# Kernel optimization log

Hardware: AMD Instinct MI355X
Metric: run time of the kernel (lower is better)

Reference implementation:

```python
import jax, jax.numpy as jnp
import numpy as np

B, N, D, D_OUT = 8, 2048, 1024, 1024

def setup_inputs() -> dict:
    key = jax.random.key(0)
    k1, k2, k3, k4, k5 = jax.random.split(key, 5)
    x = jax.random.normal(k1, (B, N, D), dtype=jnp.float32)
    # nn.Linear params: weight [out, in], bias [out]
    W_attn = jax.random.normal(k2, (D, D), dtype=jnp.float32) / np.sqrt(D)
    b_attn = jax.random.normal(k3, (D,), dtype=jnp.float32) * 0.01
    W_out = jax.random.normal(k4, (D_OUT, D), dtype=jnp.float32) / np.sqrt(D)
    b_out = jax.random.normal(k5, (D_OUT,), dtype=jnp.float32) * 0.01
    return {"x": x, "W_attn": W_attn, "b_attn": b_attn, "W_out": W_out, "b_out": b_out}

def reference(x, W_attn, b_attn, W_out, b_out):
    # query = x; key = attention_linear(x); value = output_linear(x)
    key = jnp.einsum('bnd,kd->bnk', x, W_attn) + b_attn   # [B,N,D]
    value = jnp.einsum('bnd,od->bno', x, W_out) + b_out   # [B,N,D_OUT]
    scale = 1.0 / np.sqrt(x.shape[-1]).astype(np.float32)
    scores = jnp.einsum('bqd,bkd->bqk', x, key) * scale   # [B,N,N]
    attn = jax.nn.softmax(scores, axis=-1)
    return jnp.einsum('bqk,bko->bqo', attn, value)        # [B,N,D_OUT]
```

## Files before the change

### kernel.cpp

```cpp
#include <hip/hip_runtime.h>
#include <hip/hip_bf16.h>
#include <cstdio>

typedef __bf16 bf16_t;
typedef __bf16 bf16x8 __attribute__((ext_vector_type(8)));
typedef __bf16 bf16x4 __attribute__((ext_vector_type(4)));
typedef float  f32x16 __attribute__((ext_vector_type(16)));

#define TM 128
#define TN 128
#define BK 32

__global__ __launch_bounds__(256)
void cvt_all(const float* __restrict__ x,  bf16_t* __restrict__ xb,  int nX,
             const float* __restrict__ Wa, bf16_t* __restrict__ Wab,
             const float* __restrict__ Wo, bf16_t* __restrict__ Wob, int nW)
{
    const int nT = nX + 2 * nW;
    for (int i = (blockIdx.x * 256 + threadIdx.x) * 4; i < nT; i += gridDim.x * 256 * 4) {
        const float* src; bf16_t* dst; int off;
        if (i < nX)            { src = x;  dst = xb;  off = i; }
        else if (i < nX + nW)  { src = Wa; dst = Wab; off = i - nX; }
        else                   { src = Wo; dst = Wob; off = i - nX - nW; }
        const float4 v = *(const float4*)(src + off);
        bf16x4 o;
        o[0] = (bf16_t)v.x; o[1] = (bf16_t)v.y; o[2] = (bf16_t)v.z; o[3] = (bf16_t)v.w;
        *(bf16x4*)(dst + off) = o;
    }
}

__device__ __forceinline__ void stage_tiles(
    const bf16_t* __restrict__ Ab, const bf16_t* __restrict__ Bb,
    bf16_t* As, bf16_t* Bs, int k0, int K, int t, int w)
{
    const int src_c = (t & 3) ^ ((t >> 3) & 3);
#pragma unroll
    for (int rd = 0; rd < 2; rd++) {
        const int row = rd * 64 + (t >> 2);
        __builtin_amdgcn_global_load_lds(
            (const __attribute__((address_space(1))) void*)(Ab + (size_t)row * K + k0 + src_c * 8),
            (__attribute__((address_space(3))) void*)(&As[(rd * 64 + w * 16) * 32]), 16, 0, 0);
        __builtin_amdgcn_global_load_lds(
            (const __attribute__((address_space(1))) void*)(Bb + (size_t)row * K + k0 + src_c * 8),
            (__attribute__((address_space(3))) void*)(&Bs[(rd * 64 + w * 16) * 32]), 16, 0, 0);
    }
}

__device__ __forceinline__ int fidx(int row, int c)
{
    return row * 32 + ((c ^ ((row >> 1) & 3)) * 8);
}

#define ACC_INIT(acc)                                            \
    _Pragma("unroll") for (int i = 0; i < 2; i++)                \
    _Pragma("unroll") for (int j = 0; j < 2; j++)                \
    _Pragma("unroll") for (int e = 0; e < 16; e++) acc[i][j][e] = 0.f;

#define MAINLOOP_STEP(As, Bs)                                                     \
    {                                                                             \
        bf16x8 af[2][2], bfr[2][2];                                               \
        _Pragma("unroll") for (int ks = 0; ks < 2; ks++) {                        \
            const int c = ks * 2 + lk;                                            \
            _Pragma("unroll") for (int mt = 0; mt < 2; mt++)                      \
                af[ks][mt] = *(const bf16x8*)&As[fidx(wm * 64 + mt * 32 + lm, c)];\
            _Pragma("unroll") for (int nt = 0; nt < 2; nt++)                      \
                bfr[ks][nt] = *(const bf16x8*)&Bs[fidx(wn * 64 + nt * 32 + lm, c)];\
        }                                                                         \
        _Pragma("unroll") for (int ks = 0; ks < 2; ks++)                          \
        _Pragma("unroll") for (int mt = 0; mt < 2; mt++)                          \
        _Pragma("unroll") for (int nt = 0; nt < 2; nt++)                          \
            acc[mt][nt] = __builtin_amdgcn_mfma_f32_32x32x16_bf16(                \
                af[ks][mt], bfr[ks][nt], acc[mt][nt], 0, 0, 0);                   \
    }

__global__ __launch_bounds__(256)
void gemm_scores(const bf16_t* __restrict__ A, const bf16_t* __restrict__ Bm,
                 bf16_t* __restrict__ C, float scale, int Ncols, int K,
                 long long strideA, long long strideB, long long strideC,
                 int tiles_m, int tiles_n)
{
    __shared__ bf16_t As[TM * BK];
    __shared__ bf16_t Bs[TN * BK];

    const int t    = threadIdx.x;
    const int w    = t >> 6;
    const int lane = t & 63;
    const int wm = w >> 1, wn = w & 1;
    const int lm = lane & 31;
    const int lk = lane >> 5;

    const int per_batch = tiles_m * tiles_n;
    const int batch = blockIdx.x / per_batch;
    const int rest  = blockIdx.x % per_batch;
    const int tm    = rest % tiles_m;
    const int tn    = rest / tiles_m;

    const bf16_t* Ab = A + (size_t)batch * strideA + (size_t)tm * TM * K;
    const bf16_t* Bb = Bm + (size_t)batch * strideB + (size_t)tn * TN * K;

    f32x16 acc[2][2];
    ACC_INIT(acc)

    for (int k0 = 0; k0 < K; k0 += BK) {
        stage_tiles(Ab, Bb, As, Bs, k0, K, t, w);
        __syncthreads();
        MAINLOOP_STEP(As, Bs)
        __syncthreads();
    }

#pragma unroll
    for (int mt = 0; mt < 2; mt++)
#pragma unroll
        for (int nt = 0; nt < 2; nt++) {
            const int colg = tn * TN + wn * 64 + nt * 32 + lm;
#pragma unroll
            for (int rg = 0; rg < 4; rg++) {
                const int rowg = tm * TM + wm * 64 + mt * 32 + rg * 8 + 4 * lk;
                bf16_t* p = C + (size_t)batch * strideC + (size_t)rowg * Ncols + colg;
#pragma unroll
                for (int j = 0; j < 4; j++)
                    p[(size_t)j * Ncols] = (bf16_t)(acc[mt][nt][rg * 4 + j] * scale);
            }
        }
}

__global__ __launch_bounds__(256)
void gemm_kv(const bf16_t* __restrict__ A,
             const bf16_t* __restrict__ Wa, const bf16_t* __restrict__ Wo,
             const float* __restrict__ ba, const float* __restrict__ bo,
             bf16_t* __restrict__ key, bf16_t* __restrict__ vT,
             int Nn, int Dd, int K)
{
    __shared__ bf16_t As[TM * BK];
    __shared__ bf16_t Bs[TN * BK];

    const int t    = threadIdx.x;
    const int w    = t >> 6;
    const int lane = t & 63;
    const int wm = w >> 1, wn = w & 1;
    const int lm = lane & 31;
    const int lk = lane >> 5;

    const int tiles_m = Nn / TM;
    const int per_batch = tiles_m * 16;
    const int batch = blockIdx.x / per_batch;
    const int rest  = blockIdx.x % per_batch;
    const int tm    = rest % tiles_m;
    const int tn    = rest / tiles_m;
    const bool isK  = (tn < 8);

    const bf16_t* Ab = A + (size_t)batch * Nn * K + (size_t)tm * TM * K;
    const bf16_t* Bb = (isK ? Wa + (size_t)tn * TN * K
                            : Wo + (size_t)(tn - 8) * TN * K);
    const float* bias = isK ? ba : bo;

    f32x16 acc[2][2];
    ACC_INIT(acc)

    for (int k0 = 0; k0 < K; k0 += BK) {
        stage_tiles(Ab, Bb, As, Bs, k0, K, t, w);
        __syncthreads();
        MAINLOOP_STEP(As, Bs)
        __syncthreads();
    }

#pragma unroll
    for (int mt = 0; mt < 2; mt++)
#pragma unroll
        for (int nt = 0; nt < 2; nt++) {
            const int cw = (tn & 7) * TN + wn * 64 + nt * 32 + lm;
            const float bv = bias[cw];
#pragma unroll
            for (int rg = 0; rg < 4; rg++) {
                const int rowg = tm * TM + wm * 64 + mt * 32 + rg * 8 + 4 * lk;
                if (isK) {
                    bf16_t* p = key + (size_t)batch * Nn * Dd + (size_t)rowg * Dd + cw;
#pragma unroll
                    for (int j = 0; j < 4; j++)
                        p[(size_t)j * Dd] = (bf16_t)(acc[mt][nt][rg * 4 + j] + bv);
                } else {
                    bf16_t* p = vT + (size_t)batch * Dd * Nn + (size_t)cw * Nn + rowg;
                    bf16x4 pk;
#pragma unroll
                    for (int j = 0; j < 4; j++)
                        pk[j] = (bf16_t)(acc[mt][nt][rg * 4 + j] + bv);
                    *(bf16x4*)p = pk;
                }
            }
        }
}

__global__ __launch_bounds__(256)
void softmax_rows(bf16_t* __restrict__ S)
{
    __shared__ float red[8];
    const int t = threadIdx.x;
    const int w = t >> 6;
    const int lane = t & 63;
    bf16_t* p = S + (size_t)blockIdx.x * 2048;

    bf16x8 v = *(const bf16x8*)&p[t * 8];
    float x[8];
    float m = -1e30f;
#pragma unroll
    for (int i = 0; i < 8; i++) { x[i] = (float)v[i]; m = fmaxf(m, x[i]); }
#pragma unroll
    for (int off = 32; off >= 1; off >>= 1) m = fmaxf(m, __shfl_xor(m, off));
    if (lane == 0) red[w] = m;
    __syncthreads();
    m = fmaxf(fmaxf(red[0], red[1]), fmaxf(red[2], red[3]));

    float s = 0.f;
#pragma unroll
    for (int i = 0; i < 8; i++) { x[i] = __expf(x[i] - m); s += x[i]; }
#pragma unroll
    for (int off = 32; off >= 1; off >>= 1) s += __shfl_xor(s, off);
    if (lane == 0) red[4 + w] = s;
    __syncthreads();
    const float inv = 1.f / (red[4] + red[5] + red[6] + red[7]);

    bf16x8 o;
#pragma unroll
    for (int i = 0; i < 8; i++) o[i] = (bf16_t)(x[i] * inv);
    *(bf16x8*)&p[t * 8] = o;
}

__global__ __launch_bounds__(256)
void gemm_out(const bf16_t* __restrict__ P, const bf16_t* __restrict__ vT,
              float* __restrict__ out, int Nn, int Dd)
{
    __shared__ bf16_t As[TM * BK];
    __shared__ bf16_t Bs[TN * BK];

    const int t    = threadIdx.x;
    const int w    = t >> 6;
    const int lane = t & 63;
    const int wm = w >> 1, wn = w & 1;
    const int lm = lane & 31;
    const int lk = lane >> 5;

    const int tiles_m = Nn / TM;
    const int tiles_n = Dd / TN;
    const int per_batch = tiles_m * tiles_n;
    const int batch = blockIdx.x / per_batch;
    const int rest  = blockIdx.x % per_batch;
    const int tm    = rest % tiles_m;
    const int tn    = rest / tiles_m;

    const int K = Nn;
    const bf16_t* Ab = P + (size_t)batch * Nn * Nn + (size_t)tm * TM * K;
    const bf16_t* Bb = vT + (size_t)batch * Dd * Nn + (size_t)tn * TN * K;

    f32x16 acc[2][2];
    ACC_INIT(acc)

    for (int k0 = 0; k0 < K; k0 += BK) {
        stage_tiles(Ab, Bb, As, Bs, k0, K, t, w);
        __syncthreads();
        MAINLOOP_STEP(As, Bs)
        __syncthreads();
    }

#pragma unroll
    for (int mt = 0; mt < 2; mt++)
#pragma unroll
        for (int nt = 0; nt < 2; nt++) {
            const int colg = tn * TN + wn * 64 + nt * 32 + lm;
#pragma unroll
            for (int rg = 0; rg < 4; rg++) {
                const int rowg = tm * TM + wm * 64 + mt * 32 + rg * 8 + 4 * lk;
                float* p = out + (size_t)batch * Nn * Dd + (size_t)rowg * Dd + colg;
#pragma unroll
                for (int j = 0; j < 4; j++)
                    p[(size_t)j * Dd] = acc[mt][nt][rg * 4 + j];
            }
        }
}

extern "C" void kernel_launch(void* const* d_in, const int* in_sizes, int n_in,
                              void* d_out, int out_size, void* d_ws, size_t ws_size,
                              hipStream_t stream)
{
    const int Bn = 8, Nn = 2048, Dd = 1024;

    const float* x  = (const float*)d_in[0];
    const float* Wa = (const float*)d_in[1];
    const float* ba = (const float*)d_in[2];
    const float* Wo = (const float*)d_in[3];
    const float* bo = (const float*)d_in[4];
    float* out = (float*)d_out;

    const size_t nX = (size_t)Bn * Nn * Dd;
    const size_t nW = (size_t)Dd * Dd;
    const size_t nS = (size_t)Bn * Nn * Nn;

    bf16_t* xb  = (bf16_t*)d_ws;
    bf16_t* Wab = xb + nX;
    bf16_t* Wob = Wab + nW;
    bf16_t* key = Wob + nW;
    bf16_t* vT  = key + nX;
    bf16_t* S   = vT + nX;
    const size_t needed = (nX * 3 + nW * 2 + nS) * sizeof(bf16_t);
    if (ws_size < needed)
        fprintf(stderr, "kernel_launch: ws too small: have %zu need %zu\n", ws_size, needed);

    const dim3 blk(256);
    const long long sXN = (long long)Nn * Dd;
    const long long sS  = (long long)Nn * Nn;

    cvt_all<<<dim3(18432), blk, 0, stream>>>(x, xb, (int)nX, Wa, Wab, Wo, Wob, (int)nW);

    gemm_kv<<<dim3(Bn * 16 * 16), blk, 0, stream>>>(
        xb, Wab, Wob, ba, bo, key, vT, Nn, Dd, Dd);

    gemm_scores<<<dim3(Bn * 16 * 16), blk, 0, stream>>>(
        xb, key, S, 0.03125f, Nn, Dd, sXN, sXN, sS, 16, 16);

    softmax_rows<<<dim3(Bn * Nn), blk, 0, stream>>>(S);

    gemm_out<<<dim3(Bn * 16 * 8), blk, 0, stream>>>(
        S, vT, out, Nn, Dd);
}
```

Before: 420.9 us.

## Replace 128x128 GEMMs with 256x256 tiled, double-buffered, 8-wave pipelined GEMM core

Rewrites the three GEMMs to use a shared 256x256-tile core with 512 threads, BK=64, double-buffered LDS fed by global_load_lds, and interleaved stage/compute phases with explicit waitcnt, barriers and setprio. Block indices are remapped to group tiles across XCDs. The intent is to raise arithmetic intensity and overlap global loads with MFMA work, cutting memory traffic and sync stalls. In exchange it uses far more LDS and registers, which limits occupancy, and launches fewer blocks (256 for the output GEMM), which may leave CUs idle.

```diff
diff --git a/kernel.cpp b/kernel.cpp
--- a/kernel.cpp
+++ b/kernel.cpp
@@ -7,9 +7,7 @@
 typedef __bf16 bf16x4 __attribute__((ext_vector_type(4)));
 typedef float  f32x16 __attribute__((ext_vector_type(16)));
 
-#define TM 128
-#define TN 128
-#define BK 32
+#define TILE_E (256 * 64)
 
 __global__ __launch_bounds__(256)
 void cvt_all(const float* __restrict__ x,  bf16_t* __restrict__ xb,  int nX,
@@ -29,165 +27,223 @@
     }
 }
 
-__device__ __forceinline__ void stage_tiles(
+
+template<int K>
+__device__ __forceinline__ void stage_half(
+    const bf16_t* __restrict__ src, bf16_t* lds_tile,
+    int half, int kt, int w, int l)
+{
+    const int r0 = half * 128 + w * 8 + (l >> 3);
+    const int c8 = ((l & 7) ^ (l >> 3)) * 8;
+#pragma unroll
+    for (int rr = 0; rr < 2; rr++) {
+        __builtin_amdgcn_global_load_lds(
+            (const __attribute__((address_space(1))) void*)
+                (src + (size_t)(r0 + rr * 64) * K + (size_t)kt * 64 + c8),
+            (__attribute__((address_space(3))) void*)
+                (lds_tile + (half * 128 + rr * 64 + w * 8) * 64),
+            16, 0, 0);
+    }
+}
+
+#define RDF_A(f, ks) (*(const bf16x8*)&sAc[(aoff + (f) * 32 + l31) * 64 + ((((ks) * 2 + l5) ^ lo7) * 8)])
+#define RDF_B(f, ks) (*(const bf16x8*)&sBc[(boff + (f) * 32 + l31) * 64 + ((((ks) * 2 + l5) ^ lo7) * 8)])
+
+#define MFMA_QUAD(BV, MB, NB)                                              \
+    _Pragma("unroll") for (int ks = 0; ks < 4; ks++)                       \
+    _Pragma("unroll") for (int mi = 0; mi < 2; mi++)                       \
+        acc[(MB) + mi][NB] = __builtin_amdgcn_mfma_f32_32x32x16_bf16(      \
+            ar[mi][ks], BV[ks], acc[(MB) + mi][NB], 0, 0, 0);
+
+#define LGKM0_FENCE                                        \
+    asm volatile("s_waitcnt lgkmcnt(0)" ::: "memory");     \
+    __builtin_amdgcn_sched_barrier(0);
+
+template<int K>
+__device__ __forceinline__ void gemm256_core(
     const bf16_t* __restrict__ Ab, const bf16_t* __restrict__ Bb,
-    bf16_t* As, bf16_t* Bs, int k0, int K, int t, int w)
-{
-    const int src_c = (t & 3) ^ ((t >> 3) & 3);
-#pragma unroll
-    for (int rd = 0; rd < 2; rd++) {
-        const int row = rd * 64 + (t >> 2);
-        __builtin_amdgcn_global_load_lds(
-            (const __attribute__((address_space(1))) void*)(Ab + (size_t)row * K + k0 + src_c * 8),
-            (__attribute__((address_space(3))) void*)(&As[(rd * 64 + w * 16) * 32]), 16, 0, 0);
-        __builtin_amdgcn_global_load_lds(
-            (const __attribute__((address_space(1))) void*)(Bb + (size_t)row * K + k0 + src_c * 8),
-            (__attribute__((address_space(3))) void*)(&Bs[(rd * 64 + w * 16) * 32]), 16, 0, 0);
-    }
-}
-
-__device__ __forceinline__ int fidx(int row, int c)
-{
-    return row * 32 + ((c ^ ((row >> 1) & 3)) * 8);
+    f32x16 (&acc)[4][2], int w, int l, int wm, int wn)
+{
+    __shared__ bf16_t sA[2 * TILE_E];
+    __shared__ bf16_t sB[2 * TILE_E];
+    constexpr int NKT = K / 64;
+
+    const int l31 = l & 31, l5 = l >> 5, lo7 = l & 7;
+    const int aoff = wm * 128, boff = wn * 64;
+
+    stage_half<K>(Ab, sA, 0, 0, w, l);
+    stage_half<K>(Bb, sB, 0, 0, w, l);
+    stage_half<K>(Bb, sB, 1, 0, w, l);
+    stage_half<K>(Ab, sA, 1, 0, w, l);
+    stage_half<K>(Ab, sA + TILE_E, 0, 1, w, l);
+    stage_half<K>(Bb, sB + TILE_E, 0, 1, w, l);
+    stage_half<K>(Bb, sB + TILE_E, 1, 1, w, l);
+
+    bf16x8 ar[2][4], bl[4], bh[4];
+
+#pragma unroll 2
+    for (int t = 0; t < NKT; ++t) {
+        bf16_t* sAc = sA + (t & 1) * TILE_E;
+        bf16_t* sBc = sB + (t & 1) * TILE_E;
+        bf16_t* sAn = sA + ((t + 1) & 1) * TILE_E;
+
+        if (t + 1 < NKT) { asm volatile("s_waitcnt vmcnt(6)" ::: "memory"); }
+        else             { asm volatile("s_waitcnt vmcnt(0)" ::: "memory"); }
+        __builtin_amdgcn_s_barrier();
+
+#pragma unroll
+        for (int mi = 0; mi < 2; mi++)
+#pragma unroll
+            for (int ks = 0; ks < 4; ks++) ar[mi][ks] = RDF_A(mi, ks);
+#pragma unroll
+        for (int ks = 0; ks < 4; ks++) bl[ks] = RDF_B(0, ks);
+        if (t + 1 < NKT) stage_half<K>(Ab, sAn, 1, t + 1, w, l);
+        __builtin_amdgcn_s_barrier();
+        LGKM0_FENCE
+        __builtin_amdgcn_s_setprio(1);
+        MFMA_QUAD(bl, 0, 0)
+        __builtin_amdgcn_s_setprio(0);
+        __builtin_amdgcn_s_barrier();
+
+#pragma unroll
+        for (int ks = 0; ks < 4; ks++) bh[ks] = RDF_B(1, ks);
+        __builtin_amdgcn_s_barrier();
+        LGKM0_FENCE
+        __builtin_amdgcn_s_setprio(1);
+        MFMA_QUAD(bh, 0, 1)
+        __builtin_amdgcn_s_setprio(0);
+        __builtin_amdgcn_s_barrier();
+
+#pragma unroll
+        for (int mi = 0; mi < 2; mi++)
+#pragma unroll
+            for (int ks = 0; ks < 4; ks++) ar[mi][ks] = RDF_A(2 + mi, ks);
+        if (t + 2 < NKT) stage_half<K>(Bb, sBc, 0, t + 2, w, l);
+        __builtin_amdgcn_s_barrier();
+        LGKM0_FENCE
+        __builtin_amdgcn_s_setprio(1);
+        MFMA_QUAD(bl, 2, 0)
+        __builtin_amdgcn_s_setprio(0);
+        __builtin_amdgcn_s_barrier();
+
+        if (t + 2 < NKT) {
+            stage_half<K>(Ab, sAc, 0, t + 2, w, l);
+            stage_half<K>(Bb, sBc, 1, t + 2, w, l);
+        }
+        __builtin_amdgcn_s_barrier();
+        __builtin_amdgcn_s_setprio(1);
+        MFMA_QUAD(bh, 2, 1)
+        __builtin_amdgcn_s_setprio(0);
+        __builtin_amdgcn_s_barrier();
+    }
 }
 
 #define ACC_INIT(acc)                                            \
-    _Pragma("unroll") for (int i = 0; i < 2; i++)                \
+    _Pragma("unroll") for (int i = 0; i < 4; i++)                \
     _Pragma("unroll") for (int j = 0; j < 2; j++)                \
     _Pragma("unroll") for (int e = 0; e < 16; e++) acc[i][j][e] = 0.f;
 
-#define MAINLOOP_STEP(As, Bs)                                                     \
-    {                                                                             \
-        bf16x8 af[2][2], bfr[2][2];                                               \
-        _Pragma("unroll") for (int ks = 0; ks < 2; ks++) {                        \
-            const int c = ks * 2 + lk;                                            \
-            _Pragma("unroll") for (int mt = 0; mt < 2; mt++)                      \
-                af[ks][mt] = *(const bf16x8*)&As[fidx(wm * 64 + mt * 32 + lm, c)];\
-            _Pragma("unroll") for (int nt = 0; nt < 2; nt++)                      \
-                bfr[ks][nt] = *(const bf16x8*)&Bs[fidx(wn * 64 + nt * 32 + lm, c)];\
-        }                                                                         \
-        _Pragma("unroll") for (int ks = 0; ks < 2; ks++)                          \
-        _Pragma("unroll") for (int mt = 0; mt < 2; mt++)                          \
-        _Pragma("unroll") for (int nt = 0; nt < 2; nt++)                          \
-            acc[mt][nt] = __builtin_amdgcn_mfma_f32_32x32x16_bf16(                \
-                af[ks][mt], bfr[ks][nt], acc[mt][nt], 0, 0, 0);                   \
-    }
-
-__global__ __launch_bounds__(256)
-void gemm_scores(const bf16_t* __restrict__ A, const bf16_t* __restrict__ Bm,
-                 bf16_t* __restrict__ C, float scale, int Ncols, int K,
-                 long long strideA, long long strideB, long long strideC,
-                 int tiles_m, int tiles_n)
-{
-    __shared__ bf16_t As[TM * BK];
-    __shared__ bf16_t Bs[TN * BK];
-
-    const int t    = threadIdx.x;
-    const int w    = t >> 6;
-    const int lane = t & 63;
-    const int wm = w >> 1, wn = w & 1;
-    const int lm = lane & 31;
-    const int lk = lane >> 5;
-
-    const int per_batch = tiles_m * tiles_n;
-    const int batch = blockIdx.x / per_batch;
-    const int rest  = blockIdx.x % per_batch;
-    const int tm    = rest % tiles_m;
-    const int tn    = rest / tiles_m;
-
-    const bf16_t* Ab = A + (size_t)batch * strideA + (size_t)tm * TM * K;
-    const bf16_t* Bb = Bm + (size_t)batch * strideB + (size_t)tn * TN * K;
-
-    f32x16 acc[2][2];
+__global__ __launch_bounds__(512, 2)
+void gemm_kv8(const bf16_t* __restrict__ xb,
+              const bf16_t* __restrict__ Wa, const bf16_t* __restrict__ Wo,
+              const float* __restrict__ ba, const float* __restrict__ bo,
+              bf16_t* __restrict__ key, bf16_t* __restrict__ vT)
+{
+    constexpr int K = 1024, Nn = 2048, Dd = 1024;
+    const int tid = threadIdx.x;
+    const int w = tid >> 6, l = tid & 63;
+    const int wm = w >> 2, wn = w & 3;
+
+    const int bid = blockIdx.x;
+    const int id  = (bid & 7) * 64 + (bid >> 3);
+    const int b   = id >> 6;
+    const int rest = id & 63;
+    const int tm  = rest & 7;
+    const int tn  = rest >> 3;
+    const bool isK = tn < 4;
+
+    const bf16_t* Ab = xb + (size_t)b * Nn * K + (size_t)tm * 256 * K;
+    const bf16_t* Bb = isK ? (Wa + (size_t)tn * 256 * K)
+                           : (Wo + (size_t)(tn - 4) * 256 * K);
+
+    f32x16 acc[4][2];
     ACC_INIT(acc)
-
-    for (int k0 = 0; k0 < K; k0 += BK) {
-        stage_tiles(Ab, Bb, As, Bs, k0, K, t, w);
-        __syncthreads();
-        MAINLOOP_STEP(As, Bs)
-        __syncthreads();
-    }
-
-#pragma unroll
-    for (int mt = 0; mt < 2; mt++)
-#pragma unroll
-        for (int nt = 0; nt < 2; nt++) {
-            const int colg = tn * TN + wn * 64 + nt * 32 + lm;
+    gemm256_core<K>(Ab, Bb, acc, w, l, wm, wn);
+
+    const int l31 = l & 31, l5 = l >> 5;
+    if (isK) {
+#pragma unroll
+        for (int n = 0; n < 2; n++) {
+            const int cg = (tn & 3) * 256 + wn * 64 + n * 32 + l31;
+            const float bv = ba[cg];
+#pragma unroll
+            for (int m = 0; m < 4; m++)
+#pragma unroll
+                for (int rg = 0; rg < 4; rg++) {
+                    const int rowg = tm * 256 + wm * 128 + m * 32 + rg * 8 + 4 * l5;
+                    bf16_t* p = key + (size_t)b * Nn * Dd + (size_t)rowg * Dd + cg;
+#pragma unroll
+                    for (int j = 0; j < 4; j++)
+                        p[(size_t)j * Dd] = (bf16_t)(acc[m][n][rg * 4 + j] + bv);
+                }
+        }
+    } else {
+#pragma unroll
+        for (int n = 0; n < 2; n++) {
+            const int cg = (tn & 3) * 256 + wn * 64 + n * 32 + l31;
+            const float bv = bo[cg];
+#pragma unroll
+            for (int m = 0; m < 4; m++)
+#pragma unroll
+                for (int rg = 0; rg < 4; rg++) {
+                    const int rowg = tm * 256 + wm * 128 + m * 32 + rg * 8 + 4 * l5;
+                    bf16x4 pk;
+#pragma unroll
+                    for (int j = 0; j < 4; j++) pk[j] = (bf16_t)(acc[m][n][rg * 4 + j] + bv);
+                    *(bf16x4*)(vT + (size_t)b * Dd * Nn + (size_t)cg * Nn + rowg) = pk;
+                }
+        }
+    }
+}
+
+__global__ __launch_bounds__(512, 2)
+void gemm_scores8(const bf16_t* __restrict__ xb, const bf16_t* __restrict__ key,
+                  bf16_t* __restrict__ S)
+{
+    constexpr int K = 1024, Nn = 2048;
+    const int tid = threadIdx.x;
+    const int w = tid >> 6, l = tid & 63;
+    const int wm = w >> 2, wn = w & 3;
+
+    const int bid = blockIdx.x;
+    const int id  = (bid & 7) * 64 + (bid >> 3);
+    const int b   = id >> 6;
+    const int rest = id & 63;
+    const int tm  = rest & 7;
+    const int tn  = rest >> 3;
+
+    const bf16_t* Ab = xb  + (size_t)b * Nn * K + (size_t)tm * 256 * K;
+    const bf16_t* Bb = key + (size_t)b * Nn * K + (size_t)tn * 256 * K;
+
+    f32x16 acc[4][2];
+    ACC_INIT(acc)
+    gemm256_core<K>(Ab, Bb, acc, w, l, wm, wn);
+
+    const int l31 = l & 31, l5 = l >> 5;
+#pragma unroll
+    for (int n = 0; n < 2; n++) {
+        const int cg = tn * 256 + wn * 64 + n * 32 + l31;
+#pragma unroll
+        for (int m = 0; m < 4; m++)
 #pragma unroll
             for (int rg = 0; rg < 4; rg++) {
-                const int rowg = tm * TM + wm * 64 + mt * 32 + rg * 8 + 4 * lk;
-                bf16_t* p = C + (size_t)batch * strideC + (size_t)rowg * Ncols + colg;
+                const int rowg = tm * 256 + wm * 128 + m * 32 + rg * 8 + 4 * l5;
+                bf16_t* p = S + (size_t)b * Nn * Nn + (size_t)rowg * Nn + cg;
 #pragma unroll
                 for (int j = 0; j < 4; j++)
-                    p[(size_t)j * Ncols] = (bf16_t)(acc[mt][nt][rg * 4 + j] * scale);
+                    p[(size_t)j * Nn] = (bf16_t)(acc[m][n][rg * 4 + j] * 0.03125f);
             }
-        }
-}
-
-__global__ __launch_bounds__(256)
-void gemm_kv(const bf16_t* __restrict__ A,
-             const bf16_t* __restrict__ Wa, const bf16_t* __restrict__ Wo,
-             const float* __restrict__ ba, const float* __restrict__ bo,
-             bf16_t* __restrict__ key, bf16_t* __restrict__ vT,
-             int Nn, int Dd, int K)
-{
-    __shared__ bf16_t As[TM * BK];
-    __shared__ bf16_t Bs[TN * BK];
-
-    const int t    = threadIdx.x;
-    const int w    = t >> 6;
-    const int lane = t & 63;
-    const int wm = w >> 1, wn = w & 1;
-    const int lm = lane & 31;
-    const int lk = lane >> 5;
-
-    const int tiles_m = Nn / TM;
-    const int per_batch = tiles_m * 16;
-    const int batch = blockIdx.x / per_batch;
-    const int rest  = blockIdx.x % per_batch;
-    const int tm    = rest % tiles_m;
-    const int tn    = rest / tiles_m;
-    const bool isK  = (tn < 8);
-
-    const bf16_t* Ab = A + (size_t)batch * Nn * K + (size_t)tm * TM * K;
-    const bf16_t* Bb = (isK ? Wa + (size_t)tn * TN * K
-                            : Wo + (size_t)(tn - 8) * TN * K);
-    const float* bias = isK ? ba : bo;
-
-    f32x16 acc[2][2];
-    ACC_INIT(acc)
-
-    for (int k0 = 0; k0 < K; k0 += BK) {
-        stage_tiles(Ab, Bb, As, Bs, k0, K, t, w);
-        __syncthreads();
-        MAINLOOP_STEP(As, Bs)
-        __syncthreads();
-    }
-
-#pragma unroll
-    for (int mt = 0; mt < 2; mt++)
-#pragma unroll
-        for (int nt = 0; nt < 2; nt++) {
-            const int cw = (tn & 7) * TN + wn * 64 + nt * 32 + lm;
-            const float bv = bias[cw];
-#pragma unroll
-            for (int rg = 0; rg < 4; rg++) {
-                const int rowg = tm * TM + wm * 64 + mt * 32 + rg * 8 + 4 * lk;
-                if (isK) {
-                    bf16_t* p = key + (size_t)batch * Nn * Dd + (size_t)rowg * Dd + cw;
-#pragma unroll
-                    for (int j = 0; j < 4; j++)
-                        p[(size_t)j * Dd] = (bf16_t)(acc[mt][nt][rg * 4 + j] + bv);
-                } else {
-                    bf16_t* p = vT + (size_t)batch * Dd * Nn + (size_t)cw * Nn + rowg;
-                    bf16x4 pk;
-#pragma unroll
-                    for (int j = 0; j < 4; j++)
-                        pk[j] = (bf16_t)(acc[mt][nt][rg * 4 + j] + bv);
-                    *(bf16x4*)p = pk;
-                }
-            }
-        }
+    }
 }
 
 __global__ __launch_bounds__(256)
@@ -225,56 +281,44 @@
     *(bf16x8*)&p[t * 8] = o;
 }
 
-__global__ __launch_bounds__(256)
-void gemm_out(const bf16_t* __restrict__ P, const bf16_t* __restrict__ vT,
-              float* __restrict__ out, int Nn, int Dd)
-{
-    __shared__ bf16_t As[TM * BK];
-    __shared__ bf16_t Bs[TN * BK];
-
-    const int t    = threadIdx.x;
-    const int w    = t >> 6;
-    const int lane = t & 63;
-    const int wm = w >> 1, wn = w & 1;
-    const int lm = lane & 31;
-    const int lk = lane >> 5;
-
-    const int tiles_m = Nn / TM;
-    const int tiles_n = Dd / TN;
-    const int per_batch = tiles_m * tiles_n;
-    const int batch = blockIdx.x / per_batch;
-    const int rest  = blockIdx.x % per_batch;
-    const int tm    = rest % tiles_m;
-    const int tn    = rest / tiles_m;
-
-    const int K = Nn;
-    const bf16_t* Ab = P + (size_t)batch * Nn * Nn + (size_t)tm * TM * K;
-    const bf16_t* Bb = vT + (size_t)batch * Dd * Nn + (size_t)tn * TN * K;
-
-    f32x16 acc[2][2];
+__global__ __launch_bounds__(512, 2)
+void gemm_out8(const bf16_t* __restrict__ P, const bf16_t* __restrict__ vT,
+               float* __restrict__ out)
+{
+    constexpr int K = 2048, Nn = 2048, Dd = 1024;
+    const int tid = threadIdx.x;
+    const int w = tid >> 6, l = tid & 63;
+    const int wm = w >> 2, wn = w & 3;
+
+    const int bid = blockIdx.x;
+    const int id  = (bid & 7) * 32 + (bid >> 3);
+    const int b   = id >> 5;
+    const int rest = id & 31;
+    const int tm  = rest & 7;
+    const int tn  = rest >> 3;
+
+    const bf16_t* Ab = P  + (size_t)b * Nn * Nn + (size_t)tm * 256 * Nn;
+    const bf16_t* Bb = vT + (size_t)b * Dd * Nn + (size_t)tn * 256 * Nn;
+
+    f32x16 acc[4][2];
     ACC_INIT(acc)
-
-    for (int k0 = 0; k0 < K; k0 += BK) {
-        stage_tiles(Ab, Bb, As, Bs, k0, K, t, w);
-        __syncthreads();
-        MAINLOOP_STEP(As, Bs)
-        __syncthreads();
-    }
-
-#pragma unroll
-    for (int mt = 0; mt < 2; mt++)
-#pragma unroll
-        for (int nt = 0; nt < 2; nt++) {
-            const int colg = tn * TN + wn * 64 + nt * 32 + lm;
+    gemm256_core<K>(Ab, Bb, acc, w, l, wm, wn);
+
+    const int l31 = l & 31, l5 = l >> 5;
+#pragma unroll
+    for (int n = 0; n < 2; n++) {
+        const int cg = tn * 256 + wn * 64 + n * 32 + l31;
+#pragma unroll
+        for (int m = 0; m < 4; m++)
 #pragma unroll
             for (int rg = 0; rg < 4; rg++) {
-                const int rowg = tm * TM + wm * 64 + mt * 32 + rg * 8 + 4 * lk;
-                float* p = out + (size_t)batch * Nn * Dd + (size_t)rowg * Dd + colg;
+                const int rowg = tm * 256 + wm * 128 + m * 32 + rg * 8 + 4 * l5;
+                float* p = out + (size_t)b * Nn * Dd + (size_t)rowg * Dd + cg;
 #pragma unroll
                 for (int j = 0; j < 4; j++)
-                    p[(size_t)j * Dd] = acc[mt][nt][rg * 4 + j];
+                    p[(size_t)j * Dd] = acc[m][n][rg * 4 + j];
             }
-        }
+    }
 }
 
 extern "C" void kernel_launch(void* const* d_in, const int* in_sizes, int n_in,
@@ -304,20 +348,13 @@
     if (ws_size < needed)
         fprintf(stderr, "kernel_launch: ws too small: have %zu need %zu\n", ws_size, needed);
 
-    const dim3 blk(256);
-    const long long sXN = (long long)Nn * Dd;
-    const long long sS  = (long long)Nn * Nn;
-
-    cvt_all<<<dim3(18432), blk, 0, stream>>>(x, xb, (int)nX, Wa, Wab, Wo, Wob, (int)nW);
-
-    gemm_kv<<<dim3(Bn * 16 * 16), blk, 0, stream>>>(
-        xb, Wab, Wob, ba, bo, key, vT, Nn, Dd, Dd);
-
-    gemm_scores<<<dim3(Bn * 16 * 16), blk, 0, stream>>>(
-        xb, key, S, 0.03125f, Nn, Dd, sXN, sXN, sS, 16, 16);
-
-    softmax_rows<<<dim3(Bn * Nn), blk, 0, stream>>>(S);
-
-    gemm_out<<<dim3(Bn * 16 * 8), blk, 0, stream>>>(
-        S, vT, out, Nn, Dd);
-}
+    cvt_all<<<dim3(18432), dim3(256), 0, stream>>>(x, xb, (int)nX, Wa, Wab, Wo, Wob, (int)nW);
+
+    gemm_kv8<<<dim3(512), dim3(512), 0, stream>>>(xb, Wab, Wob, ba, bo, key, vT);
+
+    gemm_scores8<<<dim3(512), dim3(512), 0, stream>>>(xb, key, S);
+
+    softmax_rows<<<dim3(Bn * Nn), dim3(256), 0, stream>>>(S);
+
+    gemm_out8<<<dim3(256), dim3(512), 0, stream>>>(S, vT, out);
+}
```

New measurement: 377.3 us. 10.4% less time.
